# Kernel tuning notes

Hardware: AMD Instinct MI355X
Metric: run time of the kernel (lower is better)

The kernel has to match this reference:

```python
import jax, jax.numpy as jnp
import numpy as np

B_, T_, D_MODEL = 2, 1024, 1024
D_STATE, D_CONV, EXPAND = 16, 4, 2
D_INNER = D_MODEL * EXPAND


def setup_inputs() -> dict:
    key = jax.random.key(0)
    ks = jax.random.split(key, 12)
    def s(k, shape, sc=0.02):
        return jax.random.normal(k, shape, jnp.float32) * sc
    return {
        "x": jax.random.normal(ks[0], (B_, T_, D_MODEL), jnp.float32),
        "ln_g": jnp.ones((D_MODEL,), jnp.float32),
        "ln_b": jnp.zeros((D_MODEL,), jnp.float32),
        "W_in": s(ks[1], (D_MODEL, 2 * D_INNER)),
        "b_in": s(ks[2], (2 * D_INNER,)),
        "conv_w": s(ks[3], (D_INNER, 1, D_CONV)),  # depthwise kernel, torch OIH layout
        "conv_b": s(ks[4], (D_INNER,)),
        "A": s(ks[5], (D_INNER, D_STATE), 0.1),
        "W_B": s(ks[6], (D_INNER, D_STATE)),
        "b_B": s(ks[7], (D_STATE,)),
        "W_C": s(ks[8], (D_INNER, D_STATE)),
        "b_C": s(ks[9], (D_STATE,)),
        "D": jnp.ones((D_INNER,), jnp.float32),
        "W_out": s(ks[10], (D_INNER, D_MODEL)),
        "b_out": s(ks[11], (D_MODEL,)),
    }


def _ssm_forward(x, ln_g, ln_b, W_in, b_in, conv_w, conv_b, A, W_B, b_B, W_C, b_C, D, W_out, b_out):
    eps = 1e-5
    # LayerNorm (biased variance, as in torch)
    mu = jnp.mean(x, axis=-1, keepdims=True)
    var = jnp.var(x, axis=-1, keepdims=True)
    xn = (x - mu) / jnp.sqrt(var + eps) * ln_g + ln_b
    # in_proj -> split into x path and gate
    proj = xn @ W_in + b_in                      # (b, t, 2*d_inner)
    xp, gate = jnp.split(proj, 2, axis=-1)
    # depthwise causal conv1d (padding=d_conv-1 on the left == torch pad + truncate)
    xc = jax.lax.conv_general_dilated(
        xp.transpose(0, 2, 1), conv_w,
        window_strides=(1,), padding=[(D_CONV - 1, 0)],
        dimension_numbers=("NCH", "OIH", "NCH"),
        feature_group_count=D_INNER,
    ).transpose(0, 2, 1) + conv_b                # (b, t, d_inner)
    xc = jax.nn.silu(xc)
    Bt = xc @ W_B + b_B                          # (b, t, d_state)
    Ct = xc @ W_C + b_C                          # (b, t, d_state)
    a = jax.nn.sigmoid(A)                        # (d_inner, d_state), per-channel decay
    u = Bt[:, :, None, :] * xc[:, :, :, None]    # (b, t, d_inner, d_state)
    a_full = jnp.broadcast_to(a, u.shape)
    # h_t = a * h_{t-1} + u_t  via first-order-recurrence associative scan
    def combine(c1, c2):
        a1, u1 = c1
        a2, u2 = c2
        return a2 * a1, a2 * u1 + u2
    _, h = jax.lax.associative_scan(combine, (a_full, u), axis=1)
    y = jnp.einsum("btns,bts->btn", h, Ct) + D * xc
    y = y * jax.nn.silu(gate)
    return y @ W_out + b_out + x                 # residual (dropout is identity in eval)


def reference(x, ln_g, ln_b, W_in, b_in, conv_w, conv_b, A, W_B, b_B, W_C, b_C, D, W_out, b_out):
    return _ssm_forward(x, ln_g, ln_b, W_in, b_in, conv_w, conv_b, A, W_B, b_B, W_C, b_C, D, W_out, b_out)
```

## Files before the change

kernel.cpp:

```cpp
#include <hip/hip_runtime.h>
#include <hip/hip_bf16.h>
#include <stdint.h>

using u16 = unsigned short;
typedef short bf16x8 __attribute__((ext_vector_type(8)));
typedef float f32x4 __attribute__((ext_vector_type(4)));

__device__ __forceinline__ float b2f(u16 u) {
  union { unsigned int i; float f; } v; v.i = ((unsigned int)u) << 16; return v.f;
}
__device__ __forceinline__ u16 f2b(float f) {
  __hip_bfloat16 h = __float2bfloat16(f);
  u16 r; __builtin_memcpy(&r, &h, 2); return r;
}
__device__ __forceinline__ bool probe_bf16(const void* p) {
  return *(const unsigned int*)p == 0x3F803F80u;
}
__device__ __forceinline__ float loadf(const void* p, size_t i, bool bf) {
  return bf ? b2f(((const u16*)p)[i]) : ((const float*)p)[i];
}
__device__ __forceinline__ void gload_lds16(const u16* g, u16* l) {
  __builtin_amdgcn_global_load_lds(
      (const __attribute__((address_space(1))) unsigned int*)(g),
      (__attribute__((address_space(3))) unsigned int*)(l),
      16, 0, 0);
}
template <int BK>
__device__ __forceinline__ int swkey(int row) {
  if constexpr (BK == 32) return (row >> 1) & 3;
  else return row & (BK / 8 - 1);
}

__device__ __forceinline__ void do_transpose(const void* __restrict__ in, u16* __restrict__ out,
                                             int R, int C, int bx, int by, int tid, bool bf) {
  __shared__ u16 tile[32][33];
  int c0 = bx * 32, r0 = by * 32;
  int tx = tid & 31, ty = tid >> 5;
#pragma unroll
  for (int i = 0; i < 4; i++) {
    size_t idx = (size_t)(r0 + ty + i * 8) * C + c0 + tx;
    tile[ty + i * 8][tx] = bf ? ((const u16*)in)[idx] : f2b(((const float*)in)[idx]);
  }
  __syncthreads();
#pragma unroll
  for (int i = 0; i < 4; i++)
    out[(size_t)(c0 + ty + i * 8) * R + r0 + tx] = tile[tx][ty + i * 8];
}

__launch_bounds__(256)
__global__ void prep_ln_kernel(const void* __restrict__ W_in, u16* __restrict__ WinT,
                               const void* __restrict__ W_out, u16* __restrict__ WoutT,
                               const void* __restrict__ WB, const void* __restrict__ WC,
                               u16* __restrict__ WTbc, const void* __restrict__ x,
                               const void* __restrict__ g, const void* __restrict__ b,
                               u16* __restrict__ xn) {
  const bool bf = probe_bf16(g);
  const int bid = blockIdx.x, tid = threadIdx.x;
  if (bid < 4096) {
    do_transpose(W_in, WinT, 1024, 4096, bid & 127, bid >> 7, tid, bf);
  } else if (bid < 6144) {
    int b2 = bid - 4096;
    do_transpose(W_out, WoutT, 2048, 1024, b2 & 31, b2 >> 5, tid, bf);
  } else if (bid < 6176) {
    int gg = (bid - 6144) * 256 + tid;
    int c = gg >> 8, k0 = (gg & 255) * 8;
    const void* W = (c < 16) ? WB : WC;
    int cc = c & 15;
    u16 pk[8];
#pragma unroll
    for (int e = 0; e < 8; e++)
      pk[e] = bf ? ((const u16*)W)[(size_t)(k0 + e) * 16 + cc]
                 : f2b(((const float*)W)[(size_t)(k0 + e) * 16 + cc]);
    *(int4*)(WTbc + (size_t)c * 2048 + k0) = *(int4*)pk;
  } else {
    const int row = bid - 6176;
    const size_t base = (size_t)row * 1024;
    float v[4]; float s = 0.f, s2 = 0.f;
#pragma unroll
    for (int i = 0; i < 4; i++) {
      v[i] = loadf(x, base + tid + i * 256, bf);
      s += v[i]; s2 += v[i] * v[i];
    }
#pragma unroll
    for (int m = 32; m >= 1; m >>= 1) { s += __shfl_xor(s, m); s2 += __shfl_xor(s2, m); }
    __shared__ float rs[4], rs2[4];
    if ((tid & 63) == 0) { rs[tid >> 6] = s; rs2[tid >> 6] = s2; }
    __syncthreads();
    s = rs[0] + rs[1] + rs[2] + rs[3];
    s2 = rs2[0] + rs2[1] + rs2[2] + rs2[3];
    float mu = s * (1.f / 1024.f);
    float var = s2 * (1.f / 1024.f) - mu * mu;
    float rstd = rsqrtf(var + 1e-5f);
#pragma unroll
    for (int i = 0; i < 4; i++) {
      int c = tid + i * 256;
      float o = (v[i] - mu) * rstd * loadf(g, c, bf) + loadf(b, c, bf);
      xn[base + c] = f2b(o);
    }
  }
}

template <int ROWS, int BK>
__device__ __forceinline__ void stage_tile(const u16* __restrict__ g, u16* lbuf,
                                           int K, int wave, int lane) {
  constexpr int LPR = BK / 8;
  constexpr int RPI = 512 / BK;
  constexpr int NI = ROWS / RPI;
  const int lr = lane / LPR, lc = lane % LPR;
#pragma unroll
  for (int j = wave; j < NI; j += 4) {
    int row = j * RPI + lr;
    int col = (lc ^ swkey<BK>(row)) * 8;
    gload_lds16(g + (size_t)row * K + col, lbuf + (size_t)j * RPI * BK);
  }
}

template <int BM, int BN, int BK, bool PARTIAL>
__launch_bounds__(256)
__global__ void gemm_async(const u16* __restrict__ A, const u16* __restrict__ BT,
                           const void* __restrict__ bias, void* __restrict__ Cout,
                           float* __restrict__ Cpart, int M, int N, int K, int k_len,
                           const void* __restrict__ probe) {
  constexpr int WM = BM / 2, WN = BN / 2;
  constexpr int TM = WM / 16, TN = WN / 16;
  constexpr int KF = BK / 32;
  __shared__ __align__(16) u16 lds[2][(BM + BN) * BK];
  const int tid = threadIdx.x;
  const int bm = blockIdx.x, bn = blockIdx.y, bz = blockIdx.z;
  const int lane = tid & 63, wave = tid >> 6;
  const int wm = wave >> 1, wn = wave & 1;
  const int lrow = lane & 15, quad = lane >> 4;
  f32x4 acc[TM][TN] = {};
  const u16* Ag = A + (size_t)bm * BM * K + (size_t)bz * k_len;
  const u16* Bg = BT + (size_t)bn * BN * K + (size_t)bz * k_len;

  stage_tile<BM, BK>(Ag, &lds[0][0], K, wave, lane);
  stage_tile<BN, BK>(Bg, &lds[0][BM * BK], K, wave, lane);
  __syncthreads();

  int cur = 0;
  for (int k0 = 0; k0 < k_len; k0 += BK, cur ^= 1) {
    if (k0 + BK < k_len) {
      stage_tile<BM, BK>(Ag + k0 + BK, &lds[cur ^ 1][0], K, wave, lane);
      stage_tile<BN, BK>(Bg + k0 + BK, &lds[cur ^ 1][BM * BK], K, wave, lane);
    }
    const u16* bufA = &lds[cur][0];
    const u16* bufB = &lds[cur][BM * BK];
#pragma unroll
    for (int f = 0; f < KF; f++) {
      bf16x8 af[TM], bv[TN];
#pragma unroll
      for (int i = 0; i < TM; i++) {
        int row = wm * WM + i * 16 + lrow;
        af[i] = *(const bf16x8*)&bufA[(size_t)row * BK + (((f * 4 + quad) ^ swkey<BK>(row)) * 8)];
      }
#pragma unroll
      for (int j = 0; j < TN; j++) {
        int row = wn * WN + j * 16 + lrow;
        bv[j] = *(const bf16x8*)&bufB[(size_t)row * BK + (((f * 4 + quad) ^ swkey<BK>(row)) * 8)];
      }
#pragma unroll
      for (int i = 0; i < TM; i++)
#pragma unroll
        for (int j = 0; j < TN; j++)
          acc[i][j] = __builtin_amdgcn_mfma_f32_16x16x32_bf16(af[i], bv[j], acc[i][j], 0, 0, 0);
    }
    __syncthreads();
  }

  if constexpr (PARTIAL) {
    float* P = Cpart + (size_t)bz * M * N;
#pragma unroll
    for (int i = 0; i < TM; i++)
#pragma unroll
      for (int j = 0; j < TN; j++) {
        int col = bn * BN + wn * WN + j * 16 + lrow;
#pragma unroll
        for (int r = 0; r < 4; r++) {
          int row = bm * BM + wm * WM + i * 16 + quad * 4 + r;
          P[(size_t)row * N + col] = acc[i][j][r];
        }
      }
    return;
  }

  const bool bf = probe_bf16(probe);
#pragma unroll
  for (int i = 0; i < TM; i++) {
#pragma unroll
    for (int j = 0; j < TN; j++) {
      int col = bn * BN + wn * WN + j * 16 + lrow;
      float bvv = loadf(bias, col, bf);
#pragma unroll
      for (int r = 0; r < 4; r++) {
        int row = bm * BM + wm * WM + i * 16 + quad * 4 + r;
        ((u16*)Cout)[(size_t)row * N + col] = f2b(acc[i][j][r] + bvv);
      }
    }
  }
}

__launch_bounds__(256)
__global__ void reduce_out(const float* __restrict__ p, const void* __restrict__ bias,
                           const void* __restrict__ resid, void* __restrict__ out,
                           const void* __restrict__ probe) {
  const bool bf = probe_bf16(probe);
  const int row = blockIdx.x, c0 = threadIdx.x * 4;
  const size_t i = (size_t)row * 1024 + c0;
  f32x4 a = *(const f32x4*)(p + i);
  f32x4 b = *(const f32x4*)(p + (size_t)2048 * 1024 + i);
  float o[4];
#pragma unroll
  for (int e = 0; e < 4; e++)
    o[e] = a[e] + b[e] + loadf(bias, c0 + e, bf) + loadf(resid, i + e, bf);
  if (bf) {
    u16 pk[4];
#pragma unroll
    for (int e = 0; e < 4; e++) pk[e] = f2b(o[e]);
    *(uint2*)((u16*)out + i) = *(uint2*)pk;
  } else {
    f32x4 v; v[0] = o[0]; v[1] = o[1]; v[2] = o[2]; v[3] = o[3];
    *(f32x4*)((float*)out + i) = v;
  }
}

__launch_bounds__(256)
__global__ void gemm_bc_conv(const u16* __restrict__ proj, const void* __restrict__ cw,
                             const void* __restrict__ cb, const u16* __restrict__ WT,
                             u16* __restrict__ xcb, float* __restrict__ part,
                             const void* __restrict__ probe) {
  const bool bf = probe_bf16(probe);
  __shared__ __align__(16) u16 lA[128 * 128];
  __shared__ __align__(16) u16 lB[32 * 128];
  const int tid = threadIdx.x;
  const int bm = blockIdx.x, bz = blockIdx.y;
  const int lane = tid & 63, wave = tid >> 6;
  const int lrow = lane & 15, quad = lane >> 4;

  stage_tile<32, 128>(WT + bz * 128, lB, 2048, wave, lane);

  const int kb = tid & 15;
  const int ch0 = bz * 128 + kb * 8;
  float wgt[8][4], bia[8];
#pragma unroll
  for (int e = 0; e < 8; e++) {
    bia[e] = loadf(cb, ch0 + e, bf);
#pragma unroll
    for (int k = 0; k < 4; k++) wgt[e][k] = loadf(cw, (size_t)(ch0 + e) * 4 + k, bf);
  }
#pragma unroll
  for (int i = 0; i < 8; i++) {
    int slot = tid + i * 256;
    int r = slot >> 4;
    int grow = bm * 128 + r;
    int t = grow & 1023;
    float acc[8];
#pragma unroll
    for (int e = 0; e < 8; e++) acc[e] = bia[e];
#pragma unroll
    for (int k = 0; k < 4; k++) {
      if (t - 3 + k >= 0) {
        union { int4 v; u16 u[8]; } uu;
        uu.v = *(const int4*)(proj + (size_t)(grow - 3 + k) * 4096 + ch0);
#pragma unroll
        for (int e = 0; e < 8; e++)
          acc[e] = __builtin_fmaf(b2f(uu.u[e]), wgt[e][k], acc[e]);
      }
    }
    union { int4 v; u16 u[8]; } pk;
#pragma unroll
    for (int e = 0; e < 8; e++) {
      float s = acc[e];
      pk.u[e] = f2b(s / (1.f + __expf(-s)));
    }
    *(int4*)(xcb + (size_t)grow * 2048 + ch0) = pk.v;
    *(int4*)&lA[r * 128 + ((kb ^ (r & 15)) * 8)] = pk.v;
  }
  __syncthreads();

  f32x4 acc[2][2] = {};
#pragma unroll
  for (int f = 0; f < 4; f++) {
    bf16x8 af[2], bv[2];
#pragma unroll
    for (int i = 0; i < 2; i++) {
      int row = wave * 32 + i * 16 + lrow;
      af[i] = *(const bf16x8*)&lA[(size_t)row * 128 + (((f * 4 + quad) ^ (row & 15)) * 8)];
    }
#pragma unroll
    for (int j = 0; j < 2; j++) {
      int row = j * 16 + lrow;
      bv[j] = *(const bf16x8*)&lB[(size_t)row * 128 + (((f * 4 + quad) ^ (row & 15)) * 8)];
    }
#pragma unroll
    for (int i = 0; i < 2; i++)
#pragma unroll
      for (int j = 0; j < 2; j++)
        acc[i][j] = __builtin_amdgcn_mfma_f32_16x16x32_bf16(af[i], bv[j], acc[i][j], 0, 0, 0);
  }
#pragma unroll
  for (int i = 0; i < 2; i++)
#pragma unroll
    for (int j = 0; j < 2; j++) {
      int col = j * 16 + lrow;
#pragma unroll
      for (int r = 0; r < 4; r++) {
        int row = bm * 128 + wave * 32 + i * 16 + quad * 4 + r;
        part[((size_t)bz * 2048 + row) * 32 + col] = acc[i][j][r];
      }
    }
}

__launch_bounds__(256)
__global__ void reduce_bc(const float* __restrict__ part, const void* __restrict__ bB,
                          const void* __restrict__ bC, float* __restrict__ BC,
                          const void* __restrict__ probe) {
  const bool bf = probe_bf16(probe);
  const int g = blockIdx.x * 256 + threadIdx.x;
  const int c = g & 31;
  float s = (c < 16) ? loadf(bB, c, bf) : loadf(bC, c - 16, bf);
#pragma unroll
  for (int z = 0; z < 16; z++) s += part[(size_t)z * 65536 + g];
  BC[g] = s;
}

__launch_bounds__(256)
__global__ void scan_pass1(const u16* __restrict__ xc, const float* __restrict__ BC,
                           const void* __restrict__ Abuf, float* __restrict__ carry,
                           const void* __restrict__ probe) {
  const bool bf = probe_bf16(probe);
  const int tid = threadIdx.x;
  const int c = blockIdx.x & 31, ng = (blockIdx.x >> 5) & 7, bi = blockIdx.x >> 8;
  const int n = ng * 256 + tid;
  float a[16], h[16];
#pragma unroll
  for (int s = 0; s < 16; s++) {
    float av = loadf(Abuf, n * 16 + s, bf);
    a[s] = 1.f / (1.f + __expf(-av));
    h[s] = 0.f;
  }
  __shared__ __align__(16) u16 xs[32 * 256];
  __shared__ __align__(16) float bcs[32 * 32];
  const u16* xcp = xc + (size_t)bi * 1024 * 2048 + ng * 256;
  const float* bcp = BC + (size_t)bi * 1024 * 32;
  const int tc = c * 32;
#pragma unroll
  for (int i = 0; i < 4; i++) {
    int ch = tid + i * 256;
    int r = ch >> 5, cv = (ch & 31) * 8;
    *(int4*)&xs[ch * 8] = *(const int4*)(xcp + (size_t)(tc + r) * 2048 + cv);
  }
  {
    int r = tid >> 3, cv = (tid & 7) * 4;
    *(int4*)&bcs[tid * 4] = *(const int4*)(bcp + (size_t)(tc + r) * 32 + cv);
  }
  __syncthreads();
  for (int t = 0; t < 32; t++) {
    float x = b2f(xs[t * 256 + tid]);
#pragma unroll
    for (int s = 0; s < 16; s++)
      h[s] = __builtin_fmaf(a[s], h[s], bcs[t * 32 + s] * x);
  }
  float* cp = carry + ((size_t)(bi * 32 + c) * 2048 + n) * 16;
#pragma unroll
  for (int s = 0; s < 16; s++) cp[s] = h[s];
}

__launch_bounds__(256)
__global__ void scan_prefix(float* __restrict__ carry, const void* __restrict__ Abuf,
                            const void* __restrict__ probe) {
  const bool bf = probe_bf16(probe);
  const int g = blockIdx.x * 256 + threadIdx.x;
  const int s = g & 15, n = (g >> 4) & 2047, bi = g >> 15;
  float a = 1.f / (1.f + __expf(-loadf(Abuf, n * 16 + s, bf)));
  float aL = a;
#pragma unroll
  for (int i = 0; i < 5; i++) aL = aL * aL;
  float running = 0.f;
  for (int c = 0; c < 32; c++) {
    size_t idx = ((size_t)(bi * 32 + c) * 2048 + n) * 16 + s;
    float tmp = carry[idx];
    carry[idx] = running;
    running = __builtin_fmaf(aL, running, tmp);
  }
}

__launch_bounds__(256)
__global__ void scan_pass2(const u16* __restrict__ xc, const u16* __restrict__ proj,
                           const float* __restrict__ BC, const void* __restrict__ Abuf,
                           const void* __restrict__ Dbuf, const float* __restrict__ carry,
                           u16* __restrict__ ybar, const void* __restrict__ probe) {
  const bool bf = probe_bf16(probe);
  const int tid = threadIdx.x;
  const int c = blockIdx.x & 31, ng = (blockIdx.x >> 5) & 7, bi = blockIdx.x >> 8;
  const int n = ng * 256 + tid;
  float a[16], h[16];
  const float* cp = carry + ((size_t)(bi * 32 + c) * 2048 + n) * 16;
#pragma unroll
  for (int s = 0; s < 16; s++) {
    float av = loadf(Abuf, n * 16 + s, bf);
    a[s] = 1.f / (1.f + __expf(-av));
    h[s] = cp[s];
  }
  const float Dn = loadf(Dbuf, n, bf);
  __shared__ __align__(16) u16 xs[32 * 256];
  __shared__ __align__(16) u16 gs[32 * 256];
  __shared__ __align__(16) float bcs[32 * 32];
  const u16* xcp = xc + (size_t)bi * 1024 * 2048 + ng * 256;
  const u16* gp = proj + (size_t)bi * 1024 * 4096 + 2048 + ng * 256;
  const float* bcp = BC + (size_t)bi * 1024 * 32;
  u16* yp = ybar + (size_t)bi * 1024 * 2048 + ng * 256;
  const int tc = c * 32;
#pragma unroll
  for (int i = 0; i < 4; i++) {
    int ch = tid + i * 256;
    int r = ch >> 5, cv = (ch & 31) * 8;
    *(int4*)&xs[ch * 8] = *(const int4*)(xcp + (size_t)(tc + r) * 2048 + cv);
    *(int4*)&gs[ch * 8] = *(const int4*)(gp + (size_t)(tc + r) * 4096 + cv);
  }
  {
    int r = tid >> 3, cv = (tid & 7) * 4;
    *(int4*)&bcs[tid * 4] = *(const int4*)(bcp + (size_t)(tc + r) * 32 + cv);
  }
  __syncthreads();
  for (int t = 0; t < 32; t++) {
    float x = b2f(xs[t * 256 + tid]);
    float acc = 0.f;
#pragma unroll
    for (int s = 0; s < 16; s++) {
      h[s] = __builtin_fmaf(a[s], h[s], bcs[t * 32 + s] * x);
      acc = __builtin_fmaf(h[s], bcs[t * 32 + 16 + s], acc);
    }
    float y = acc + Dn * x;
    float g = b2f(gs[t * 256 + tid]);
    float yg = y * g / (1.f + __expf(-g));
    yp[(size_t)(tc + t) * 2048 + tid] = f2b(yg);
  }
}

extern "C" void kernel_launch(void* const* d_in, const int* in_sizes, int n_in,
                              void* d_out, int out_size, void* d_ws, size_t ws_size,
                              hipStream_t stream) {
  const void* x = d_in[0];
  const void* ln_g = d_in[1];
  const void* ln_b = d_in[2];
  const void* W_in = d_in[3];
  const void* b_in = d_in[4];
  const void* conv_w = d_in[5];
  const void* conv_b = d_in[6];
  const void* A = d_in[7];
  const void* W_B = d_in[8];
  const void* b_B = d_in[9];
  const void* W_C = d_in[10];
  const void* b_C = d_in[11];
  const void* Dp = d_in[12];
  const void* W_out = d_in[13];
  const void* b_out = d_in[14];
  const void* probe = ln_g;

  char* ws = (char*)d_ws;
  u16* WinT = (u16*)ws;
  u16* ybar = (u16*)ws;
  u16* xn = (u16*)(ws + (size_t)8 * 1024 * 1024);
  u16* proj = (u16*)(ws + (size_t)12 * 1024 * 1024);
  u16* xcb = (u16*)(ws + (size_t)28 * 1024 * 1024);
  float* BC = (float*)(ws + (size_t)36 * 1024 * 1024);
  float* carry = (float*)(ws + (size_t)36 * 1024 * 1024 + 256 * 1024);
  u16* WTbc = (u16*)(ws + (size_t)46 * 1024 * 1024);
  float* part = (float*)(ws + (size_t)48 * 1024 * 1024);
  u16* WoutT = (u16*)(ws + (size_t)64 * 1024 * 1024);
  float* part_bc = (float*)(ws + (size_t)68 * 1024 * 1024);

  prep_ln_kernel<<<8224, 256, 0, stream>>>(W_in, WinT, W_out, WoutT, W_B, W_C, WTbc,
                                           x, ln_g, ln_b, xn);
  gemm_async<128, 128, 64, false><<<dim3(16, 32), 256, 0, stream>>>(
      xn, WinT, b_in, proj, nullptr, 2048, 4096, 1024, 1024, probe);
  gemm_bc_conv<<<dim3(16, 16), 256, 0, stream>>>(proj, conv_w, conv_b, WTbc,
                                                 xcb, part_bc, probe);
  reduce_bc<<<256, 256, 0, stream>>>(part_bc, b_B, b_C, BC, probe);
  scan_pass1<<<512, 256, 0, stream>>>(xcb, BC, A, carry, probe);
  scan_prefix<<<256, 256, 0, stream>>>(carry, A, probe);
  scan_pass2<<<512, 256, 0, stream>>>(xcb, proj, BC, A, Dp, carry, ybar, probe);
  gemm_async<128, 64, 64, true><<<dim3(16, 16, 2), 256, 0, stream>>>(
      ybar, WoutT, nullptr, nullptr, part, 2048, 1024, 2048, 1024, probe);
  reduce_out<<<2048, 256, 0, stream>>>(part, b_out, x, d_out, probe);
}
```

Baseline: 207.0 us.

## Fuse split-K reductions into scan kernels and out-proj GEMM epilogue

Removes the reduce_bc kernel by having each scan pass sum the 16 split-K partials for its B/C tile directly into shared memory. Replaces the split-K out-projection plus reduce_out with a single 64x64-tile GEMM whose epilogue adds bias and residual and writes bf16 or fp32 output. This cuts two launches and the fp32 partial-buffer round trips through memory. In exchange the scans redo the B/C reduction (once per channel group and pass), and the out-proj GEMM uses smaller tiles with a full-K loop per block.

```diff
diff --git a/kernel.cpp b/kernel.cpp
--- a/kernel.cpp
+++ b/kernel.cpp
@@ -115,32 +115,32 @@
   }
 }
 
-template <int BM, int BN, int BK, bool PARTIAL>
+template <int BM, int BN, int BK, bool RESID, bool DUALOUT>
 __launch_bounds__(256)
 __global__ void gemm_async(const u16* __restrict__ A, const u16* __restrict__ BT,
-                           const void* __restrict__ bias, void* __restrict__ Cout,
-                           float* __restrict__ Cpart, int M, int N, int K, int k_len,
+                           const void* __restrict__ bias, const void* __restrict__ resid,
+                           void* __restrict__ Cout, int M, int N, int K,
                            const void* __restrict__ probe) {
   constexpr int WM = BM / 2, WN = BN / 2;
   constexpr int TM = WM / 16, TN = WN / 16;
   constexpr int KF = BK / 32;
   __shared__ __align__(16) u16 lds[2][(BM + BN) * BK];
   const int tid = threadIdx.x;
-  const int bm = blockIdx.x, bn = blockIdx.y, bz = blockIdx.z;
+  const int bm = blockIdx.x, bn = blockIdx.y;
   const int lane = tid & 63, wave = tid >> 6;
   const int wm = wave >> 1, wn = wave & 1;
   const int lrow = lane & 15, quad = lane >> 4;
   f32x4 acc[TM][TN] = {};
-  const u16* Ag = A + (size_t)bm * BM * K + (size_t)bz * k_len;
-  const u16* Bg = BT + (size_t)bn * BN * K + (size_t)bz * k_len;
+  const u16* Ag = A + (size_t)bm * BM * K;
+  const u16* Bg = BT + (size_t)bn * BN * K;
 
   stage_tile<BM, BK>(Ag, &lds[0][0], K, wave, lane);
   stage_tile<BN, BK>(Bg, &lds[0][BM * BK], K, wave, lane);
   __syncthreads();
 
   int cur = 0;
-  for (int k0 = 0; k0 < k_len; k0 += BK, cur ^= 1) {
-    if (k0 + BK < k_len) {
+  for (int k0 = 0; k0 < K; k0 += BK, cur ^= 1) {
+    if (k0 + BK < K) {
       stage_tile<BM, BK>(Ag + k0 + BK, &lds[cur ^ 1][0], K, wave, lane);
       stage_tile<BN, BK>(Bg + k0 + BK, &lds[cur ^ 1][BM * BK], K, wave, lane);
     }
@@ -168,22 +168,6 @@
     __syncthreads();
   }
 
-  if constexpr (PARTIAL) {
-    float* P = Cpart + (size_t)bz * M * N;
-#pragma unroll
-    for (int i = 0; i < TM; i++)
-#pragma unroll
-      for (int j = 0; j < TN; j++) {
-        int col = bn * BN + wn * WN + j * 16 + lrow;
-#pragma unroll
-        for (int r = 0; r < 4; r++) {
-          int row = bm * BM + wm * WM + i * 16 + quad * 4 + r;
-          P[(size_t)row * N + col] = acc[i][j][r];
-        }
-      }
-    return;
-  }
-
   const bool bf = probe_bf16(probe);
 #pragma unroll
   for (int i = 0; i < TM; i++) {
@@ -194,33 +178,16 @@
 #pragma unroll
       for (int r = 0; r < 4; r++) {
         int row = bm * BM + wm * WM + i * 16 + quad * 4 + r;
-        ((u16*)Cout)[(size_t)row * N + col] = f2b(acc[i][j][r] + bvv);
+        float v = acc[i][j][r] + bvv;
+        if constexpr (RESID) v += loadf(resid, (size_t)row * N + col, bf);
+        if constexpr (DUALOUT) {
+          if (bf) ((u16*)Cout)[(size_t)row * N + col] = f2b(v);
+          else    ((float*)Cout)[(size_t)row * N + col] = v;
+        } else {
+          ((u16*)Cout)[(size_t)row * N + col] = f2b(v);
+        }
       }
     }
-  }
-}
-
-__launch_bounds__(256)
-__global__ void reduce_out(const float* __restrict__ p, const void* __restrict__ bias,
-                           const void* __restrict__ resid, void* __restrict__ out,
-                           const void* __restrict__ probe) {
-  const bool bf = probe_bf16(probe);
-  const int row = blockIdx.x, c0 = threadIdx.x * 4;
-  const size_t i = (size_t)row * 1024 + c0;
-  f32x4 a = *(const f32x4*)(p + i);
-  f32x4 b = *(const f32x4*)(p + (size_t)2048 * 1024 + i);
-  float o[4];
-#pragma unroll
-  for (int e = 0; e < 4; e++)
-    o[e] = a[e] + b[e] + loadf(bias, c0 + e, bf) + loadf(resid, i + e, bf);
-  if (bf) {
-    u16 pk[4];
-#pragma unroll
-    for (int e = 0; e < 4; e++) pk[e] = f2b(o[e]);
-    *(uint2*)((u16*)out + i) = *(uint2*)pk;
-  } else {
-    f32x4 v; v[0] = o[0]; v[1] = o[1]; v[2] = o[2]; v[3] = o[3];
-    *(f32x4*)((float*)out + i) = v;
   }
 }
 
@@ -311,27 +278,32 @@
     }
 }
 
-__launch_bounds__(256)
-__global__ void reduce_bc(const float* __restrict__ part, const void* __restrict__ bB,
-                          const void* __restrict__ bC, float* __restrict__ BC,
-                          const void* __restrict__ probe) {
-  const bool bf = probe_bf16(probe);
-  const int g = blockIdx.x * 256 + threadIdx.x;
-  const int c = g & 31;
-  float s = (c < 16) ? loadf(bB, c, bf) : loadf(bC, c - 16, bf);
-#pragma unroll
-  for (int z = 0; z < 16; z++) s += part[(size_t)z * 65536 + g];
-  BC[g] = s;
-}
-
-__launch_bounds__(256)
-__global__ void scan_pass1(const u16* __restrict__ xc, const float* __restrict__ BC,
+__device__ __forceinline__ void bc_tile_reduce(const float* __restrict__ part_bc,
+                                               const void* __restrict__ bB,
+                                               const void* __restrict__ bC,
+                                               float* bcs, int bi, int tc, int tid, bool bf) {
+#pragma unroll
+  for (int e = 0; e < 4; e++) {
+    int idx = tid * 4 + e;
+    int tt = idx >> 5, cc = idx & 31;
+    size_t grow = (size_t)bi * 1024 + tc + tt;
+    float s = (cc < 16) ? loadf(bB, cc, bf) : loadf(bC, cc - 16, bf);
+#pragma unroll
+    for (int z = 0; z < 16; z++) s += part_bc[(size_t)z * 65536 + grow * 32 + cc];
+    bcs[idx] = s;
+  }
+}
+
+__launch_bounds__(256)
+__global__ void scan_pass1(const u16* __restrict__ xc, const float* __restrict__ part_bc,
+                           const void* __restrict__ bB, const void* __restrict__ bC,
                            const void* __restrict__ Abuf, float* __restrict__ carry,
                            const void* __restrict__ probe) {
   const bool bf = probe_bf16(probe);
   const int tid = threadIdx.x;
   const int c = blockIdx.x & 31, ng = (blockIdx.x >> 5) & 7, bi = blockIdx.x >> 8;
   const int n = ng * 256 + tid;
+  const int tc = c * 32;
   float a[16], h[16];
 #pragma unroll
   for (int s = 0; s < 16; s++) {
@@ -342,17 +314,12 @@
   __shared__ __align__(16) u16 xs[32 * 256];
   __shared__ __align__(16) float bcs[32 * 32];
   const u16* xcp = xc + (size_t)bi * 1024 * 2048 + ng * 256;
-  const float* bcp = BC + (size_t)bi * 1024 * 32;
-  const int tc = c * 32;
+  bc_tile_reduce(part_bc, bB, bC, bcs, bi, tc, tid, bf);
 #pragma unroll
   for (int i = 0; i < 4; i++) {
     int ch = tid + i * 256;
     int r = ch >> 5, cv = (ch & 31) * 8;
     *(int4*)&xs[ch * 8] = *(const int4*)(xcp + (size_t)(tc + r) * 2048 + cv);
-  }
-  {
-    int r = tid >> 3, cv = (tid & 7) * 4;
-    *(int4*)&bcs[tid * 4] = *(const int4*)(bcp + (size_t)(tc + r) * 32 + cv);
   }
   __syncthreads();
   for (int t = 0; t < 32; t++) {
@@ -387,13 +354,15 @@
 
 __launch_bounds__(256)
 __global__ void scan_pass2(const u16* __restrict__ xc, const u16* __restrict__ proj,
-                           const float* __restrict__ BC, const void* __restrict__ Abuf,
+                           const float* __restrict__ part_bc, const void* __restrict__ bB,
+                           const void* __restrict__ bC, const void* __restrict__ Abuf,
                            const void* __restrict__ Dbuf, const float* __restrict__ carry,
                            u16* __restrict__ ybar, const void* __restrict__ probe) {
   const bool bf = probe_bf16(probe);
   const int tid = threadIdx.x;
   const int c = blockIdx.x & 31, ng = (blockIdx.x >> 5) & 7, bi = blockIdx.x >> 8;
   const int n = ng * 256 + tid;
+  const int tc = c * 32;
   float a[16], h[16];
   const float* cp = carry + ((size_t)(bi * 32 + c) * 2048 + n) * 16;
 #pragma unroll
@@ -408,19 +377,14 @@
   __shared__ __align__(16) float bcs[32 * 32];
   const u16* xcp = xc + (size_t)bi * 1024 * 2048 + ng * 256;
   const u16* gp = proj + (size_t)bi * 1024 * 4096 + 2048 + ng * 256;
-  const float* bcp = BC + (size_t)bi * 1024 * 32;
   u16* yp = ybar + (size_t)bi * 1024 * 2048 + ng * 256;
-  const int tc = c * 32;
+  bc_tile_reduce(part_bc, bB, bC, bcs, bi, tc, tid, bf);
 #pragma unroll
   for (int i = 0; i < 4; i++) {
     int ch = tid + i * 256;
     int r = ch >> 5, cv = (ch & 31) * 8;
     *(int4*)&xs[ch * 8] = *(const int4*)(xcp + (size_t)(tc + r) * 2048 + cv);
     *(int4*)&gs[ch * 8] = *(const int4*)(gp + (size_t)(tc + r) * 4096 + cv);
-  }
-  {
-    int r = tid >> 3, cv = (tid & 7) * 4;
-    *(int4*)&bcs[tid * 4] = *(const int4*)(bcp + (size_t)(tc + r) * 32 + cv);
   }
   __syncthreads();
   for (int t = 0; t < 32; t++) {
@@ -464,24 +428,21 @@
   u16* xn = (u16*)(ws + (size_t)8 * 1024 * 1024);
   u16* proj = (u16*)(ws + (size_t)12 * 1024 * 1024);
   u16* xcb = (u16*)(ws + (size_t)28 * 1024 * 1024);
-  float* BC = (float*)(ws + (size_t)36 * 1024 * 1024);
   float* carry = (float*)(ws + (size_t)36 * 1024 * 1024 + 256 * 1024);
   u16* WTbc = (u16*)(ws + (size_t)46 * 1024 * 1024);
-  float* part = (float*)(ws + (size_t)48 * 1024 * 1024);
   u16* WoutT = (u16*)(ws + (size_t)64 * 1024 * 1024);
   float* part_bc = (float*)(ws + (size_t)68 * 1024 * 1024);
 
   prep_ln_kernel<<<8224, 256, 0, stream>>>(W_in, WinT, W_out, WoutT, W_B, W_C, WTbc,
                                            x, ln_g, ln_b, xn);
-  gemm_async<128, 128, 64, false><<<dim3(16, 32), 256, 0, stream>>>(
-      xn, WinT, b_in, proj, nullptr, 2048, 4096, 1024, 1024, probe);
+  gemm_async<128, 128, 64, false, false><<<dim3(16, 32), 256, 0, stream>>>(
+      xn, WinT, b_in, nullptr, proj, 2048, 4096, 1024, probe);
   gemm_bc_conv<<<dim3(16, 16), 256, 0, stream>>>(proj, conv_w, conv_b, WTbc,
                                                  xcb, part_bc, probe);
-  reduce_bc<<<256, 256, 0, stream>>>(part_bc, b_B, b_C, BC, probe);
-  scan_pass1<<<512, 256, 0, stream>>>(xcb, BC, A, carry, probe);
+  scan_pass1<<<512, 256, 0, stream>>>(xcb, part_bc, b_B, b_C, A, carry, probe);
   scan_prefix<<<256, 256, 0, stream>>>(carry, A, probe);
-  scan_pass2<<<512, 256, 0, stream>>>(xcb, proj, BC, A, Dp, carry, ybar, probe);
-  gemm_async<128, 64, 64, true><<<dim3(16, 16, 2), 256, 0, stream>>>(
-      ybar, WoutT, nullptr, nullptr, part, 2048, 1024, 2048, 1024, probe);
-  reduce_out<<<2048, 256, 0, stream>>>(part, b_out, x, d_out, probe);
-}
+  scan_pass2<<<512, 256, 0, stream>>>(xcb, proj, part_bc, b_B, b_C, A, Dp, carry,
+                                      ybar, probe);
+  gemm_async<64, 64, 64, true, true><<<dim3(32, 16), 256, 0, stream>>>(
+      ybar, WoutT, b_out, x, d_out, 2048, 1024, 2048, probe);
+}
```

Measured after the change: 219.5 us. 6.1% more time.

## Fuse split-K reductions into GEMM epilogues via last-block atomic counters

Applied to the files above, without the earlier changes.

Removes the separate reduce_bc and reduce_out kernels by having each split-K block publish its partial tile and increment an atomic counter; the last-arriving block for a tile sums the other partials and applies bias/residual. Counters are zeroed by an extra block in the prep kernel. This saves two kernel launches and one read of the partials for the output GEMM, at the cost of atomic synchronization and a serial tail in the finishing blocks.

```diff
diff --git a/kernel.cpp b/kernel.cpp
--- a/kernel.cpp
+++ b/kernel.cpp
@@ -25,6 +25,12 @@
       (__attribute__((address_space(3))) unsigned int*)(l),
       16, 0, 0);
 }
+__device__ __forceinline__ void cstore(float* p, float v) {
+  __hip_atomic_store(p, v, __ATOMIC_RELAXED, __HIP_MEMORY_SCOPE_AGENT);
+}
+__device__ __forceinline__ float cload(const float* p) {
+  return __hip_atomic_load(p, __ATOMIC_RELAXED, __HIP_MEMORY_SCOPE_AGENT);
+}
 template <int BK>
 __device__ __forceinline__ int swkey(int row) {
   if constexpr (BK == 32) return (row >> 1) & 3;
@@ -53,7 +59,7 @@
                                const void* __restrict__ WB, const void* __restrict__ WC,
                                u16* __restrict__ WTbc, const void* __restrict__ x,
                                const void* __restrict__ g, const void* __restrict__ b,
-                               u16* __restrict__ xn) {
+                               u16* __restrict__ xn, int* __restrict__ counters) {
   const bool bf = probe_bf16(g);
   const int bid = blockIdx.x, tid = threadIdx.x;
   if (bid < 4096) {
@@ -72,7 +78,7 @@
       pk[e] = bf ? ((const u16*)W)[(size_t)(k0 + e) * 16 + cc]
                  : f2b(((const float*)W)[(size_t)(k0 + e) * 16 + cc]);
     *(int4*)(WTbc + (size_t)c * 2048 + k0) = *(int4*)pk;
-  } else {
+  } else if (bid < 8224) {
     const int row = bid - 6176;
     const size_t base = (size_t)row * 1024;
     float v[4]; float s = 0.f, s2 = 0.f;
@@ -97,6 +103,9 @@
       float o = (v[i] - mu) * rstd * loadf(g, c, bf) + loadf(b, c, bf);
       xn[base + c] = f2b(o);
     }
+  } else {
+    for (int i = tid; i < 272; i += 256)
+      __hip_atomic_store(&counters[i], 0, __ATOMIC_RELAXED, __HIP_MEMORY_SCOPE_AGENT);
   }
 }
 
@@ -115,15 +124,81 @@
   }
 }
 
-template <int BM, int BN, int BK, bool PARTIAL>
+template <int BM, int BN, int BK>
 __launch_bounds__(256)
 __global__ void gemm_async(const u16* __restrict__ A, const u16* __restrict__ BT,
-                           const void* __restrict__ bias, void* __restrict__ Cout,
-                           float* __restrict__ Cpart, int M, int N, int K, int k_len,
-                           const void* __restrict__ probe) {
+                           const void* __restrict__ bias, u16* __restrict__ Cout,
+                           int M, int N, int K, const void* __restrict__ probe) {
   constexpr int WM = BM / 2, WN = BN / 2;
   constexpr int TM = WM / 16, TN = WN / 16;
   constexpr int KF = BK / 32;
+  __shared__ __align__(16) u16 lds[2][(BM + BN) * BK];
+  const int tid = threadIdx.x;
+  const int bm = blockIdx.x, bn = blockIdx.y;
+  const int lane = tid & 63, wave = tid >> 6;
+  const int wm = wave >> 1, wn = wave & 1;
+  const int lrow = lane & 15, quad = lane >> 4;
+  f32x4 acc[TM][TN] = {};
+  const u16* Ag = A + (size_t)bm * BM * K;
+  const u16* Bg = BT + (size_t)bn * BN * K;
+
+  stage_tile<BM, BK>(Ag, &lds[0][0], K, wave, lane);
+  stage_tile<BN, BK>(Bg, &lds[0][BM * BK], K, wave, lane);
+  __syncthreads();
+
+  int cur = 0;
+  for (int k0 = 0; k0 < K; k0 += BK, cur ^= 1) {
+    if (k0 + BK < K) {
+      stage_tile<BM, BK>(Ag + k0 + BK, &lds[cur ^ 1][0], K, wave, lane);
+      stage_tile<BN, BK>(Bg + k0 + BK, &lds[cur ^ 1][BM * BK], K, wave, lane);
+    }
+    const u16* bufA = &lds[cur][0];
+    const u16* bufB = &lds[cur][BM * BK];
+#pragma unroll
+    for (int f = 0; f < KF; f++) {
+      bf16x8 af[TM], bv[TN];
+#pragma unroll
+      for (int i = 0; i < TM; i++) {
+        int row = wm * WM + i * 16 + lrow;
+        af[i] = *(const bf16x8*)&bufA[(size_t)row * BK + (((f * 4 + quad) ^ swkey<BK>(row)) * 8)];
+      }
+#pragma unroll
+      for (int j = 0; j < TN; j++) {
+        int row = wn * WN + j * 16 + lrow;
+        bv[j] = *(const bf16x8*)&bufB[(size_t)row * BK + (((f * 4 + quad) ^ swkey<BK>(row)) * 8)];
+      }
+#pragma unroll
+      for (int i = 0; i < TM; i++)
+#pragma unroll
+        for (int j = 0; j < TN; j++)
+          acc[i][j] = __builtin_amdgcn_mfma_f32_16x16x32_bf16(af[i], bv[j], acc[i][j], 0, 0, 0);
+    }
+    __syncthreads();
+  }
+
+  const bool bf = probe_bf16(probe);
+#pragma unroll
+  for (int i = 0; i < TM; i++) {
+#pragma unroll
+    for (int j = 0; j < TN; j++) {
+      int col = bn * BN + wn * WN + j * 16 + lrow;
+      float bvv = loadf(bias, col, bf);
+#pragma unroll
+      for (int r = 0; r < 4; r++) {
+        int row = bm * BM + wm * WM + i * 16 + quad * 4 + r;
+        Cout[(size_t)row * N + col] = f2b(acc[i][j][r] + bvv);
+      }
+    }
+  }
+}
+
+__launch_bounds__(256)
+__global__ void gemm_out(const u16* __restrict__ A, const u16* __restrict__ BT,
+                         const void* __restrict__ bias, const void* __restrict__ resid,
+                         float* __restrict__ part, int* __restrict__ counters,
+                         void* __restrict__ out, const void* __restrict__ probe) {
+  constexpr int BM = 128, BN = 64, BK = 64, KLEN = 1024;
+  constexpr int WM = 64, WN = 32, TM = 4, TN = 2, KF = 2;
   __shared__ __align__(16) u16 lds[2][(BM + BN) * BK];
   const int tid = threadIdx.x;
   const int bm = blockIdx.x, bn = blockIdx.y, bz = blockIdx.z;
@@ -131,18 +206,17 @@
   const int wm = wave >> 1, wn = wave & 1;
   const int lrow = lane & 15, quad = lane >> 4;
   f32x4 acc[TM][TN] = {};
-  const u16* Ag = A + (size_t)bm * BM * K + (size_t)bz * k_len;
-  const u16* Bg = BT + (size_t)bn * BN * K + (size_t)bz * k_len;
-
-  stage_tile<BM, BK>(Ag, &lds[0][0], K, wave, lane);
-  stage_tile<BN, BK>(Bg, &lds[0][BM * BK], K, wave, lane);
-  __syncthreads();
-
+  const u16* Ag = A + (size_t)bm * BM * 2048 + (size_t)bz * KLEN;
+  const u16* Bg = BT + (size_t)bn * BN * 2048 + (size_t)bz * KLEN;
+
+  stage_tile<BM, BK>(Ag, &lds[0][0], 2048, wave, lane);
+  stage_tile<BN, BK>(Bg, &lds[0][BM * BK], 2048, wave, lane);
+  __syncthreads();
   int cur = 0;
-  for (int k0 = 0; k0 < k_len; k0 += BK, cur ^= 1) {
-    if (k0 + BK < k_len) {
-      stage_tile<BM, BK>(Ag + k0 + BK, &lds[cur ^ 1][0], K, wave, lane);
-      stage_tile<BN, BK>(Bg + k0 + BK, &lds[cur ^ 1][BM * BK], K, wave, lane);
+  for (int k0 = 0; k0 < KLEN; k0 += BK, cur ^= 1) {
+    if (k0 + BK < KLEN) {
+      stage_tile<BM, BK>(Ag + k0 + BK, &lds[cur ^ 1][0], 2048, wave, lane);
+      stage_tile<BN, BK>(Bg + k0 + BK, &lds[cur ^ 1][BM * BK], 2048, wave, lane);
     }
     const u16* bufA = &lds[cur][0];
     const u16* bufB = &lds[cur][BM * BK];
@@ -168,23 +242,28 @@
     __syncthreads();
   }
 
-  if constexpr (PARTIAL) {
-    float* P = Cpart + (size_t)bz * M * N;
-#pragma unroll
-    for (int i = 0; i < TM; i++)
-#pragma unroll
-      for (int j = 0; j < TN; j++) {
-        int col = bn * BN + wn * WN + j * 16 + lrow;
-#pragma unroll
-        for (int r = 0; r < 4; r++) {
-          int row = bm * BM + wm * WM + i * 16 + quad * 4 + r;
-          P[(size_t)row * N + col] = acc[i][j][r];
-        }
-      }
-    return;
-  }
+  float* P = part + (size_t)bz * 2048 * 1024;
+#pragma unroll
+  for (int i = 0; i < TM; i++)
+#pragma unroll
+    for (int j = 0; j < TN; j++) {
+      int col = bn * BN + wn * WN + j * 16 + lrow;
+#pragma unroll
+      for (int r = 0; r < 4; r++) {
+        int row = bm * BM + wm * WM + i * 16 + quad * 4 + r;
+        cstore(&P[(size_t)row * 1024 + col], acc[i][j][r]);
+      }
+    }
+  __syncthreads();
+  __shared__ int lastv;
+  if (tid == 0)
+    lastv = __hip_atomic_fetch_add(&counters[16 + bm * 16 + bn], 1,
+                                   __ATOMIC_ACQ_REL, __HIP_MEMORY_SCOPE_AGENT);
+  __syncthreads();
+  if (lastv != 1) return;
 
   const bool bf = probe_bf16(probe);
+  const float* Q = part + (size_t)(bz ^ 1) * 2048 * 1024;
 #pragma unroll
   for (int i = 0; i < TM; i++) {
 #pragma unroll
@@ -194,40 +273,21 @@
 #pragma unroll
       for (int r = 0; r < 4; r++) {
         int row = bm * BM + wm * WM + i * 16 + quad * 4 + r;
-        ((u16*)Cout)[(size_t)row * N + col] = f2b(acc[i][j][r] + bvv);
-      }
-    }
-  }
-}
-
-__launch_bounds__(256)
-__global__ void reduce_out(const float* __restrict__ p, const void* __restrict__ bias,
-                           const void* __restrict__ resid, void* __restrict__ out,
-                           const void* __restrict__ probe) {
-  const bool bf = probe_bf16(probe);
-  const int row = blockIdx.x, c0 = threadIdx.x * 4;
-  const size_t i = (size_t)row * 1024 + c0;
-  f32x4 a = *(const f32x4*)(p + i);
-  f32x4 b = *(const f32x4*)(p + (size_t)2048 * 1024 + i);
-  float o[4];
-#pragma unroll
-  for (int e = 0; e < 4; e++)
-    o[e] = a[e] + b[e] + loadf(bias, c0 + e, bf) + loadf(resid, i + e, bf);
-  if (bf) {
-    u16 pk[4];
-#pragma unroll
-    for (int e = 0; e < 4; e++) pk[e] = f2b(o[e]);
-    *(uint2*)((u16*)out + i) = *(uint2*)pk;
-  } else {
-    f32x4 v; v[0] = o[0]; v[1] = o[1]; v[2] = o[2]; v[3] = o[3];
-    *(f32x4*)((float*)out + i) = v;
+        size_t off = (size_t)row * 1024 + col;
+        float v = acc[i][j][r] + cload(&Q[off]) + bvv + loadf(resid, off, bf);
+        if (bf) ((u16*)out)[off] = f2b(v);
+        else    ((float*)out)[off] = v;
+      }
+    }
   }
 }
 
 __launch_bounds__(256)
 __global__ void gemm_bc_conv(const u16* __restrict__ proj, const void* __restrict__ cw,
                              const void* __restrict__ cb, const u16* __restrict__ WT,
+                             const void* __restrict__ bB, const void* __restrict__ bC,
                              u16* __restrict__ xcb, float* __restrict__ part,
+                             int* __restrict__ counters, float* __restrict__ BC,
                              const void* __restrict__ probe) {
   const bool bf = probe_bf16(probe);
   __shared__ __align__(16) u16 lA[128 * 128];
@@ -306,22 +366,27 @@
 #pragma unroll
       for (int r = 0; r < 4; r++) {
         int row = bm * 128 + wave * 32 + i * 16 + quad * 4 + r;
-        part[((size_t)bz * 2048 + row) * 32 + col] = acc[i][j][r];
-      }
-    }
-}
-
-__launch_bounds__(256)
-__global__ void reduce_bc(const float* __restrict__ part, const void* __restrict__ bB,
-                          const void* __restrict__ bC, float* __restrict__ BC,
-                          const void* __restrict__ probe) {
-  const bool bf = probe_bf16(probe);
-  const int g = blockIdx.x * 256 + threadIdx.x;
-  const int c = g & 31;
-  float s = (c < 16) ? loadf(bB, c, bf) : loadf(bC, c - 16, bf);
-#pragma unroll
-  for (int z = 0; z < 16; z++) s += part[(size_t)z * 65536 + g];
-  BC[g] = s;
+        cstore(&part[((size_t)bz * 2048 + row) * 32 + col], acc[i][j][r]);
+      }
+    }
+  __syncthreads();
+  __shared__ int lastv;
+  if (tid == 0)
+    lastv = __hip_atomic_fetch_add(&counters[bm], 1,
+                                   __ATOMIC_ACQ_REL, __HIP_MEMORY_SCOPE_AGENT);
+  __syncthreads();
+  if (lastv != 15) return;
+
+#pragma unroll
+  for (int e = 0; e < 16; e++) {
+    int idx = tid + e * 256;
+    int r = idx >> 5, cc = idx & 31;
+    size_t off = ((size_t)bm * 128 + r) * 32 + cc;
+    float s = (cc < 16) ? loadf(bB, cc, bf) : loadf(bC, cc - 16, bf);
+#pragma unroll
+    for (int z = 0; z < 16; z++) s += cload(&part[(size_t)z * 65536 + off]);
+    BC[off] = s;
+  }
 }
 
 __launch_bounds__(256)
@@ -470,18 +535,17 @@
   float* part = (float*)(ws + (size_t)48 * 1024 * 1024);
   u16* WoutT = (u16*)(ws + (size_t)64 * 1024 * 1024);
   float* part_bc = (float*)(ws + (size_t)68 * 1024 * 1024);
-
-  prep_ln_kernel<<<8224, 256, 0, stream>>>(W_in, WinT, W_out, WoutT, W_B, W_C, WTbc,
-                                           x, ln_g, ln_b, xn);
-  gemm_async<128, 128, 64, false><<<dim3(16, 32), 256, 0, stream>>>(
-      xn, WinT, b_in, proj, nullptr, 2048, 4096, 1024, 1024, probe);
-  gemm_bc_conv<<<dim3(16, 16), 256, 0, stream>>>(proj, conv_w, conv_b, WTbc,
-                                                 xcb, part_bc, probe);
-  reduce_bc<<<256, 256, 0, stream>>>(part_bc, b_B, b_C, BC, probe);
+  int* counters = (int*)(ws + (size_t)72 * 1024 * 1024);
+
+  prep_ln_kernel<<<8225, 256, 0, stream>>>(W_in, WinT, W_out, WoutT, W_B, W_C, WTbc,
+                                           x, ln_g, ln_b, xn, counters);
+  gemm_async<128, 128, 64><<<dim3(16, 32), 256, 0, stream>>>(
+      xn, WinT, b_in, proj, 2048, 4096, 1024, probe);
+  gemm_bc_conv<<<dim3(16, 16), 256, 0, stream>>>(proj, conv_w, conv_b, WTbc, b_B, b_C,
+                                                 xcb, part_bc, counters, BC, probe);
   scan_pass1<<<512, 256, 0, stream>>>(xcb, BC, A, carry, probe);
   scan_prefix<<<256, 256, 0, stream>>>(carry, A, probe);
   scan_pass2<<<512, 256, 0, stream>>>(xcb, proj, BC, A, Dp, carry, ybar, probe);
-  gemm_async<128, 64, 64, true><<<dim3(16, 16, 2), 256, 0, stream>>>(
-      ybar, WoutT, nullptr, nullptr, part, 2048, 1024, 2048, 1024, probe);
-  reduce_out<<<2048, 256, 0, stream>>>(part, b_out, x, d_out, probe);
-}
+  gemm_out<<<dim3(16, 16, 2), 256, 0, stream>>>(ybar, WoutT, b_out, x, part, counters,
+                                                d_out, probe);
+}
```

After: 247.9 us. 1.2x slower.
